# Kernel optimization log

Measured on AMD Instinct MI355X. Metric: run time of the kernel, lower is better.

## Reference

```python
import jax, jax.numpy as jnp
import numpy as np

B, F, Q = 8192, 128, 64
H1, H2 = 256, 256
THRESHOLD = 0.95
EPS = 1e-12


def setup_inputs() -> dict:
    key = jax.random.key(0)
    ks = jax.random.split(key, 8)
    in_dim = F + 1 + Q  # raw + quantum + graph feature
    def lin(k, fan_in, fan_out):
        bound = 1.0 / np.sqrt(fan_in)
        kw, kb = jax.random.split(k)
        W = jax.random.uniform(kw, (fan_out, fan_in), jnp.float32, -bound, bound)
        b = jax.random.uniform(kb, (fan_out,), jnp.float32, -bound, bound)
        return W, b
    W1, b1 = lin(ks[2], in_dim, H1)
    W2, b2 = lin(ks[3], H1, H2)
    W3, b3 = lin(ks[4], H2, 1)
    return {
        'x': jax.random.normal(ks[0], (B, F), jnp.float32),
        'quantum_features': jax.random.normal(ks[1], (B, Q), jnp.float32),
        'W1': W1, 'b1': b1, 'W2': W2, 'b2': b2, 'W3': W3, 'b3': b3,
    }


def _graph_feat(x):
    # normalized Gram matrix -> squared cosine fidelity -> threshold -> row mean
    xn = x / (jnp.linalg.norm(x, axis=1, keepdims=True) + EPS)  # [B, F]
    fid = jnp.square(xn @ xn.T)                                  # [B, B]
    adj = jnp.where(fid >= THRESHOLD, 1.0, 0.0)
    adj = adj * (1.0 - jnp.eye(x.shape[0], dtype=x.dtype))       # no self-edges
    return jnp.mean(adj, axis=1, keepdims=True)                  # [B, 1]


def reference(x, quantum_features, W1, b1, W2, b2, W3, b3):
    graph_feat = jax.lax.stop_gradient(_graph_feat(x))  # built under no_grad in torch
    feats = jnp.concatenate([x, quantum_features, graph_feat], axis=1)  # [B, F+Q+1]
    h = jax.nn.relu(feats @ W1.T + b1)
    h = jax.nn.relu(h @ W2.T + b2)
    out = h @ W3.T + b3  # [B, 1]
    return out[:, 0]
```

## Files before the change

kernel.cpp:

```cpp
#include <hip/hip_runtime.h>
#include <hip/hip_bf16.h>

typedef __attribute__((ext_vector_type(8))) short bf16x8;
typedef __attribute__((ext_vector_type(4))) float f32x4;
typedef unsigned int uint;

#define NROWS 8192
#define F_DIM 128
#define Q_DIM 64
#define KPAD  224
#define H_DIM 256

static __device__ inline unsigned short bf_bits(__hip_bfloat16 b) {
  unsigned short u; __builtin_memcpy(&u, &b, 2); return u;
}
static __device__ inline uint packhl(float v) {
  __hip_bfloat16 h = __float2bfloat16(v);
  float hf = __bfloat162float(h);
  __hip_bfloat16 l = __float2bfloat16(v - hf);
  return ((uint)bf_bits(l) << 16) | (uint)bf_bits(h);
}

__global__ __launch_bounds__(256) void norm_feats_kernel(const float* __restrict__ x,
                                                         const float* __restrict__ q,
                                                         __hip_bfloat16* __restrict__ xn,
                                                         uint* __restrict__ feats_p,
                                                         int* __restrict__ cnt) {
  int tid = threadIdx.x;
  int lane = tid & 63;
  int row = blockIdx.x * 4 + (tid >> 6);
  if (blockIdx.x < 32) cnt[blockIdx.x * 256 + tid] = 0;
  const float2 v = *(const float2*)(x + (size_t)row * F_DIM + lane * 2);
  float s = v.x * v.x + v.y * v.y;
#pragma unroll
  for (int off = 32; off; off >>= 1) s += __shfl_xor(s, off);
  float inv = 1.0f / (sqrtf(s) + 1e-12f);
  __hip_bfloat162 p;
  p.x = __float2bfloat16(v.x * inv);
  p.y = __float2bfloat16(v.y * inv);
  *(__hip_bfloat162*)(xn + (size_t)row * F_DIM + lane * 2) = p;

  uint* frow = feats_p + (size_t)row * KPAD;
  uint2 u;
  u.x = packhl(v.x); u.y = packhl(v.y);
  *(uint2*)(frow + lane * 2) = u;
  if (lane < 32) {
    const float2 qv = *(const float2*)(q + (size_t)row * Q_DIM + lane * 2);
    u.x = packhl(qv.x); u.y = packhl(qv.y);
    *(uint2*)(frow + 128 + lane * 2) = u;
  } else if (lane < 48) {
    uint2 z = {0u, 0u};
    *(uint2*)(frow + 192 + (lane - 32) * 2) = z;
  }
}

__global__ __launch_bounds__(256) void prep_w_kernel(const float* __restrict__ W1,
                                                     const float* __restrict__ W2,
                                                     uint* __restrict__ W1P,
                                                     uint* __restrict__ W2P) {
  int b = blockIdx.x, k = threadIdx.x;
  if (b < 256) {
    if (k < KPAD) W1P[b * KPAD + k] = (k < 193) ? packhl(W1[b * 193 + k]) : 0u;
  } else {
    int n = b - 256;
    W2P[n * 256 + k] = packhl(W2[n * 256 + k]);
  }
}

__global__ __launch_bounds__(256) void gram_kernel(const __hip_bfloat16* __restrict__ xnp,
                                                   int* __restrict__ cnt) {
  __shared__ char smem[65536];
  const short* xn = (const short*)xnp;
  int tid = threadIdx.x;
  int lane = tid & 63;
  int wave = tid >> 6;
  int lr = lane & 15;
  int quad = lane >> 4;

  int t = blockIdx.x;
  int bi = (int)((129.0f - sqrtf(129.0f * 129.0f - 8.0f * (float)t)) * 0.5f);
  while ((bi + 1) * (129 - (bi + 1)) / 2 <= t) bi++;
  while (bi * (129 - bi) / 2 > t) bi--;
  int bj = bi + (t - bi * (129 - bi) / 2);
  int i0 = bi * 128, j0 = bj * 128;

#pragma unroll
  for (int it = 0; it < 16; ++it) {
    int half = it >> 3;
    int row = (it & 7) * 16 + (tid >> 4);
    int chunk = tid & 15;
    int grow = (half ? j0 : i0) + row;
    bf16x8 v = *(const bf16x8*)(xn + (size_t)grow * F_DIM + chunk * 8);
    *(bf16x8*)(smem + half * 32768 + row * 256 + ((chunk ^ (row & 15)) << 4)) = v;
  }
  __syncthreads();

  int wi = (wave >> 1) * 64, wj = (wave & 1) * 64;

  f32x4 acc[4][4];
#pragma unroll
  for (int i = 0; i < 4; i++)
#pragma unroll
    for (int j = 0; j < 4; j++) acc[i][j] = (f32x4){0.f, 0.f, 0.f, 0.f};

#pragma unroll
  for (int kk = 0; kk < 4; kk++) {
    int c = kk * 4 + quad;
    bf16x8 a[4], b[4];
#pragma unroll
    for (int tt = 0; tt < 4; tt++) {
      int row = wi + tt * 16 + lr;
      a[tt] = *(const bf16x8*)(smem + row * 256 + ((c ^ lr) << 4));
    }
#pragma unroll
    for (int tt = 0; tt < 4; tt++) {
      int row = wj + tt * 16 + lr;
      b[tt] = *(const bf16x8*)(smem + 32768 + row * 256 + ((c ^ lr) << 4));
    }
#pragma unroll
    for (int tr = 0; tr < 4; tr++)
#pragma unroll
      for (int tc = 0; tc < 4; tc++)
        acc[tr][tc] = __builtin_amdgcn_mfma_f32_16x16x32_bf16(a[tr], b[tc], acc[tr][tc], 0, 0, 0);
  }

  int i_base = i0 + wi, j_base = j0 + wj;
  bool diag_wave = (i_base == j_base);
  bool offdiag_block = (bi != bj);

  float mx = 0.f;
#pragma unroll
  for (int tr = 0; tr < 4; tr++)
#pragma unroll
    for (int tc = 0; tc < 4; tc++)
#pragma unroll
      for (int r = 0; r < 4; r++) {
        float v = acc[tr][tc][r];
        if (diag_wave && tr == tc && lr == quad * 4 + r) v = 0.f;
        mx = fmaxf(mx, fabsf(v));
      }
  if (__any(mx >= 0.9746f)) {
    for (int tr = 0; tr < 4; tr++)
      for (int tc = 0; tc < 4; tc++)
        for (int r = 0; r < 4; r++) {
          float v = acc[tr][tc][r];
          int row = i_base + tr * 16 + quad * 4 + r;
          int col = j_base + tc * 16 + lr;
          if (v * v >= 0.95f && row != col) {
            atomicAdd(&cnt[row], 1);
            if (offdiag_block) atomicAdd(&cnt[col], 1);
          }
        }
  }
}

__global__ __launch_bounds__(256) void gf_kernel(const int* __restrict__ cnt,
                                                 const float* __restrict__ b3,
                                                 uint* __restrict__ feats_p,
                                                 float* __restrict__ out) {
  int i = blockIdx.x * 256 + threadIdx.x;
  feats_p[(size_t)i * KPAD + 192] = packhl((float)cnt[i] * (1.0f / 8192.0f));
  out[i] = b3[0];
}

template <int K, int MODE>
__global__ __launch_bounds__(256) void gemm_mfma(const uint* __restrict__ A,
                                                 const uint* __restrict__ Bp,
                                                 const float* __restrict__ bias,
                                                 uint* __restrict__ Out,
                                                 const float* __restrict__ W3,
                                                 float* __restrict__ out) {
  __shared__ short Ahi[128 * 40];
  __shared__ short Alo[128 * 40];
  __shared__ short Bhi[64 * 40];
  __shared__ short Blo[64 * 40];

  int tid = threadIdx.x;
  int lane = tid & 63;
  int wave = tid >> 6;
  int lr = lane & 15;
  int quad = lane >> 4;
  int mb = blockIdx.x * 128;
  int nb = blockIdx.y * 64;
  int wm = (wave & 1) * 64;
  int wn = (wave >> 1) * 32;

  int a_row = tid >> 3;
  int a_c4 = (tid & 7) * 4;
  int b_row = tid >> 3;

  f32x4 acc[4][2];
#pragma unroll
  for (int i = 0; i < 4; i++)
#pragma unroll
    for (int j = 0; j < 2; j++) acc[i][j] = (f32x4){0.f, 0.f, 0.f, 0.f};

  constexpr int NIT = K / 32;
  uint4 ar[4], br[2];

#pragma unroll
  for (int i = 0; i < 4; i++)
    ar[i] = *(const uint4*)(A + (size_t)(mb + a_row + i * 32) * K + a_c4);
#pragma unroll
  for (int i = 0; i < 2; i++)
    br[i] = *(const uint4*)(Bp + (size_t)(nb + b_row + i * 32) * K + a_c4);

  for (int it = 0; it < NIT; ++it) {
    __syncthreads();
#pragma unroll
    for (int i = 0; i < 4; i++) {
      int r = a_row + i * 32;
      uint h01 = (ar[i].x & 0xffffu) | (ar[i].y << 16);
      uint h23 = (ar[i].z & 0xffffu) | (ar[i].w << 16);
      uint l01 = (ar[i].x >> 16) | (ar[i].y & 0xffff0000u);
      uint l23 = (ar[i].z >> 16) | (ar[i].w & 0xffff0000u);
      *(uint2*)&Ahi[r * 40 + a_c4] = (uint2){h01, h23};
      *(uint2*)&Alo[r * 40 + a_c4] = (uint2){l01, l23};
    }
#pragma unroll
    for (int i = 0; i < 2; i++) {
      int r = b_row + i * 32;
      uint h01 = (br[i].x & 0xffffu) | (br[i].y << 16);
      uint h23 = (br[i].z & 0xffffu) | (br[i].w << 16);
      uint l01 = (br[i].x >> 16) | (br[i].y & 0xffff0000u);
      uint l23 = (br[i].z >> 16) | (br[i].w & 0xffff0000u);
      *(uint2*)&Bhi[r * 40 + a_c4] = (uint2){h01, h23};
      *(uint2*)&Blo[r * 40 + a_c4] = (uint2){l01, l23};
    }
    __syncthreads();

    if (it + 1 < NIT) {
      int k0 = (it + 1) * 32;
#pragma unroll
      for (int i = 0; i < 4; i++)
        ar[i] = *(const uint4*)(A + (size_t)(mb + a_row + i * 32) * K + k0 + a_c4);
#pragma unroll
      for (int i = 0; i < 2; i++)
        br[i] = *(const uint4*)(Bp + (size_t)(nb + b_row + i * 32) * K + k0 + a_c4);
    }

    bf16x8 ahi[4], alo[4], bhi[2], blo[2];
#pragma unroll
    for (int tt = 0; tt < 4; tt++) {
      int r = wm + tt * 16 + lr;
      ahi[tt] = *(const bf16x8*)&Ahi[r * 40 + quad * 8];
      alo[tt] = *(const bf16x8*)&Alo[r * 40 + quad * 8];
    }
#pragma unroll
    for (int tc = 0; tc < 2; tc++) {
      int r = wn + tc * 16 + lr;
      bhi[tc] = *(const bf16x8*)&Bhi[r * 40 + quad * 8];
      blo[tc] = *(const bf16x8*)&Blo[r * 40 + quad * 8];
    }
#pragma unroll
    for (int tt = 0; tt < 4; tt++)
#pragma unroll
      for (int tc = 0; tc < 2; tc++) {
        acc[tt][tc] = __builtin_amdgcn_mfma_f32_16x16x32_bf16(ahi[tt], bhi[tc], acc[tt][tc], 0, 0, 0);
        acc[tt][tc] = __builtin_amdgcn_mfma_f32_16x16x32_bf16(ahi[tt], blo[tc], acc[tt][tc], 0, 0, 0);
        acc[tt][tc] = __builtin_amdgcn_mfma_f32_16x16x32_bf16(alo[tt], bhi[tc], acc[tt][tc], 0, 0, 0);
      }
  }

  if (MODE == 1) {
#pragma unroll
    for (int tc = 0; tc < 2; tc++) {
      int n = nb + wn + tc * 16 + lr;
      float bv = bias[n];
#pragma unroll
      for (int tt = 0; tt < 4; tt++) {
        int m0 = mb + wm + tt * 16 + quad * 4;
#pragma unroll
        for (int r = 0; r < 4; r++) {
          float v = fmaxf(acc[tt][tc][r] + bv, 0.f);
          Out[(size_t)(m0 + r) * 256 + n] = packhl(v);
        }
      }
    }
  } else {
#pragma unroll
    for (int tt = 0; tt < 4; tt++) {
      float s[4] = {0.f, 0.f, 0.f, 0.f};
#pragma unroll
      for (int tc = 0; tc < 2; tc++) {
        int n = nb + wn + tc * 16 + lr;
        float bv = bias[n];
        float w3v = W3[n];
#pragma unroll
        for (int r = 0; r < 4; r++) {
          float v = fmaxf(acc[tt][tc][r] + bv, 0.f);
          s[r] += v * w3v;
        }
      }
#pragma unroll
      for (int r = 0; r < 4; r++) {
        s[r] += __shfl_xor(s[r], 1);
        s[r] += __shfl_xor(s[r], 2);
        s[r] += __shfl_xor(s[r], 4);
        s[r] += __shfl_xor(s[r], 8);
      }
      if (lr == 0) {
        int m0 = mb + wm + tt * 16 + quad * 4;
#pragma unroll
        for (int r = 0; r < 4; r++) atomicAdd(&out[m0 + r], s[r]);
      }
    }
  }
}

extern "C" void kernel_launch(void* const* d_in, const int* in_sizes, int n_in,
                              void* d_out, int out_size, void* d_ws, size_t ws_size,
                              hipStream_t stream) {
  const float* x  = (const float*)d_in[0];
  const float* q  = (const float*)d_in[1];
  const float* W1 = (const float*)d_in[2];
  const float* b1 = (const float*)d_in[3];
  const float* W2 = (const float*)d_in[4];
  const float* b2 = (const float*)d_in[5];
  const float* W3 = (const float*)d_in[6];
  const float* b3 = (const float*)d_in[7];
  float* out = (float*)d_out;

  char* ws = (char*)d_ws;
  __hip_bfloat16* xn = (__hip_bfloat16*)(ws);
  int*  cnt     = (int*)(ws + 0x200000);
  uint* W1P     = (uint*)(ws + 0x210000);
  uint* W2P     = (uint*)(ws + 0x250000);
  uint* feats_p = (uint*)(ws + 0x290000);
  uint* h1p     = (uint*)(ws + 0x990000);

  norm_feats_kernel<<<dim3(2048), dim3(256), 0, stream>>>(x, q, xn, feats_p, cnt);
  prep_w_kernel<<<dim3(512), dim3(256), 0, stream>>>(W1, W2, W1P, W2P);
  gram_kernel<<<dim3(2080), dim3(256), 0, stream>>>(xn, cnt);
  gf_kernel<<<dim3(32), dim3(256), 0, stream>>>(cnt, b3, feats_p, out);
  gemm_mfma<KPAD, 1><<<dim3(64, 4), dim3(256), 0, stream>>>(feats_p, W1P, b1, h1p, nullptr, nullptr);
  gemm_mfma<256, 2><<<dim3(64, 4), dim3(256), 0, stream>>>(h1p, W2P, b2, nullptr, W3, out);
}
```

Baseline: 111.7 us.

## Use FP8 scaled MFMA for Gram matrix and fuse prep/gf kernels

Normalized x is now quantized to FP8 (e4m3) and the Gram kernel uses the 16x16x128 scaled f8f6f4 MFMA, halving LDS and global traffic and issuing one MFMA per tile instead of four. The weight-prep kernel is merged into the normalization kernel. The graph-feature kernel is removed: the count is injected into the first GEMM's A tile, and b3 is added in the second GEMM's epilogue after a memset of out. The goal is fewer launches and a cheaper Gram pass. The risk is FP8 precision near the 0.95 fidelity threshold, where counts could differ from the reference.

```diff
diff --git a/kernel.cpp b/kernel.cpp
--- a/kernel.cpp
+++ b/kernel.cpp
@@ -2,6 +2,7 @@
 #include <hip/hip_bf16.h>
 
 typedef __attribute__((ext_vector_type(8))) short bf16x8;
+typedef __attribute__((ext_vector_type(8))) int i32x8;
 typedef __attribute__((ext_vector_type(4))) float f32x4;
 typedef unsigned int uint;
 
@@ -21,12 +22,26 @@
   return ((uint)bf_bits(l) << 16) | (uint)bf_bits(h);
 }
 
-__global__ __launch_bounds__(256) void norm_feats_kernel(const float* __restrict__ x,
-                                                         const float* __restrict__ q,
-                                                         __hip_bfloat16* __restrict__ xn,
-                                                         uint* __restrict__ feats_p,
-                                                         int* __restrict__ cnt) {
+__global__ __launch_bounds__(256) void norm_prep_kernel(const float* __restrict__ x,
+                                                        const float* __restrict__ q,
+                                                        const float* __restrict__ W1,
+                                                        const float* __restrict__ W2,
+                                                        unsigned char* __restrict__ xn8,
+                                                        uint* __restrict__ feats_p,
+                                                        uint* __restrict__ W1P,
+                                                        uint* __restrict__ W2P,
+                                                        int* __restrict__ cnt) {
   int tid = threadIdx.x;
+  if (blockIdx.x >= 2048) {
+    int b = blockIdx.x - 2048;
+    if (b < 256) {
+      if (tid < KPAD) W1P[b * KPAD + tid] = (tid < 193) ? packhl(W1[b * 193 + tid]) : 0u;
+    } else {
+      int n = b - 256;
+      W2P[n * 256 + tid] = packhl(W2[n * 256 + tid]);
+    }
+    return;
+  }
   int lane = tid & 63;
   int row = blockIdx.x * 4 + (tid >> 6);
   if (blockIdx.x < 32) cnt[blockIdx.x * 256 + tid] = 0;
@@ -35,10 +50,8 @@
 #pragma unroll
   for (int off = 32; off; off >>= 1) s += __shfl_xor(s, off);
   float inv = 1.0f / (sqrtf(s) + 1e-12f);
-  __hip_bfloat162 p;
-  p.x = __float2bfloat16(v.x * inv);
-  p.y = __float2bfloat16(v.y * inv);
-  *(__hip_bfloat162*)(xn + (size_t)row * F_DIM + lane * 2) = p;
+  int pk = __builtin_amdgcn_cvt_pk_fp8_f32(v.x * inv, v.y * inv, 0, 0);
+  *(unsigned short*)(xn8 + (size_t)row * F_DIM + lane * 2) = (unsigned short)(pk & 0xffff);
 
   uint* frow = feats_p + (size_t)row * KPAD;
   uint2 u;
@@ -54,23 +67,9 @@
   }
 }
 
-__global__ __launch_bounds__(256) void prep_w_kernel(const float* __restrict__ W1,
-                                                     const float* __restrict__ W2,
-                                                     uint* __restrict__ W1P,
-                                                     uint* __restrict__ W2P) {
-  int b = blockIdx.x, k = threadIdx.x;
-  if (b < 256) {
-    if (k < KPAD) W1P[b * KPAD + k] = (k < 193) ? packhl(W1[b * 193 + k]) : 0u;
-  } else {
-    int n = b - 256;
-    W2P[n * 256 + k] = packhl(W2[n * 256 + k]);
-  }
-}
-
-__global__ __launch_bounds__(256) void gram_kernel(const __hip_bfloat16* __restrict__ xnp,
-                                                   int* __restrict__ cnt) {
-  __shared__ char smem[65536];
-  const short* xn = (const short*)xnp;
+__global__ __launch_bounds__(256) void gram8_kernel(const unsigned char* __restrict__ xn8,
+                                                    int* __restrict__ cnt) {
+  __shared__ char smem[32768];
   int tid = threadIdx.x;
   int lane = tid & 63;
   int wave = tid >> 6;
@@ -85,13 +84,13 @@
   int i0 = bi * 128, j0 = bj * 128;
 
 #pragma unroll
-  for (int it = 0; it < 16; ++it) {
-    int half = it >> 3;
-    int row = (it & 7) * 16 + (tid >> 4);
-    int chunk = tid & 15;
+  for (int it = 0; it < 8; ++it) {
+    int half = it >> 2;
+    int row = (it & 3) * 32 + (tid >> 3);
+    int chunk = tid & 7;
     int grow = (half ? j0 : i0) + row;
-    bf16x8 v = *(const bf16x8*)(xn + (size_t)grow * F_DIM + chunk * 8);
-    *(bf16x8*)(smem + half * 32768 + row * 256 + ((chunk ^ (row & 15)) << 4)) = v;
+    uint4 v = *(const uint4*)(xn8 + (size_t)grow * F_DIM + chunk * 16);
+    *(uint4*)(smem + half * 16384 + row * 128 + ((chunk ^ (row & 7)) << 4)) = v;
   }
   __syncthreads();
 
@@ -103,26 +102,36 @@
 #pragma unroll
     for (int j = 0; j < 4; j++) acc[i][j] = (f32x4){0.f, 0.f, 0.f, 0.f};
 
-#pragma unroll
-  for (int kk = 0; kk < 4; kk++) {
-    int c = kk * 4 + quad;
-    bf16x8 a[4], b[4];
-#pragma unroll
-    for (int tt = 0; tt < 4; tt++) {
-      int row = wi + tt * 16 + lr;
-      a[tt] = *(const bf16x8*)(smem + row * 256 + ((c ^ lr) << 4));
-    }
-#pragma unroll
-    for (int tt = 0; tt < 4; tt++) {
-      int row = wj + tt * 16 + lr;
-      b[tt] = *(const bf16x8*)(smem + 32768 + row * 256 + ((c ^ lr) << 4));
-    }
-#pragma unroll
-    for (int tr = 0; tr < 4; tr++)
-#pragma unroll
-      for (int tc = 0; tc < 4; tc++)
-        acc[tr][tc] = __builtin_amdgcn_mfma_f32_16x16x32_bf16(a[tr], b[tc], acc[tr][tc], 0, 0, 0);
-  }
+  i32x8 a[4], b[4];
+#pragma unroll
+  for (int tt = 0; tt < 4; tt++) {
+    int r = wi + tt * 16 + lr;
+    const char* base = smem + r * 128;
+    uint4 lo = *(const uint4*)(base + (((2 * quad) ^ (r & 7)) << 4));
+    uint4 hi = *(const uint4*)(base + (((2 * quad + 1) ^ (r & 7)) << 4));
+    i32x8 f;
+    f[0] = lo.x; f[1] = lo.y; f[2] = lo.z; f[3] = lo.w;
+    f[4] = hi.x; f[5] = hi.y; f[6] = hi.z; f[7] = hi.w;
+    a[tt] = f;
+  }
+#pragma unroll
+  for (int tt = 0; tt < 4; tt++) {
+    int r = wj + tt * 16 + lr;
+    const char* base = smem + 16384 + r * 128;
+    uint4 lo = *(const uint4*)(base + (((2 * quad) ^ (r & 7)) << 4));
+    uint4 hi = *(const uint4*)(base + (((2 * quad + 1) ^ (r & 7)) << 4));
+    i32x8 f;
+    f[0] = lo.x; f[1] = lo.y; f[2] = lo.z; f[3] = lo.w;
+    f[4] = hi.x; f[5] = hi.y; f[6] = hi.z; f[7] = hi.w;
+    b[tt] = f;
+  }
+
+#pragma unroll
+  for (int tr = 0; tr < 4; tr++)
+#pragma unroll
+    for (int tc = 0; tc < 4; tc++)
+      acc[tr][tc] = __builtin_amdgcn_mfma_scale_f32_16x16x128_f8f6f4(
+          a[tr], b[tc], acc[tr][tc], 0, 0, 0, 0x7f7f7f7f, 0, 0x7f7f7f7f);
 
   int i_base = i0 + wi, j_base = j0 + wj;
   bool diag_wave = (i_base == j_base);
@@ -154,21 +163,14 @@
   }
 }
 
-__global__ __launch_bounds__(256) void gf_kernel(const int* __restrict__ cnt,
-                                                 const float* __restrict__ b3,
-                                                 uint* __restrict__ feats_p,
-                                                 float* __restrict__ out) {
-  int i = blockIdx.x * 256 + threadIdx.x;
-  feats_p[(size_t)i * KPAD + 192] = packhl((float)cnt[i] * (1.0f / 8192.0f));
-  out[i] = b3[0];
-}
-
 template <int K, int MODE>
 __global__ __launch_bounds__(256) void gemm_mfma(const uint* __restrict__ A,
                                                  const uint* __restrict__ Bp,
                                                  const float* __restrict__ bias,
                                                  uint* __restrict__ Out,
                                                  const float* __restrict__ W3,
+                                                 const float* __restrict__ b3,
+                                                 const int* __restrict__ cnt,
                                                  float* __restrict__ out) {
   __shared__ short Ahi[128 * 40];
   __shared__ short Alo[128 * 40];
@@ -187,7 +189,13 @@
 
   int a_row = tid >> 3;
   int a_c4 = (tid & 7) * 4;
-  int b_row = tid >> 3;
+
+  uint gf[4];
+  if (MODE == 1 && a_c4 == 0) {
+#pragma unroll
+    for (int i = 0; i < 4; i++)
+      gf[i] = packhl((float)cnt[mb + a_row + i * 32] * (1.0f / 8192.0f));
+  }
 
   f32x4 acc[4][2];
 #pragma unroll
@@ -203,9 +211,13 @@
     ar[i] = *(const uint4*)(A + (size_t)(mb + a_row + i * 32) * K + a_c4);
 #pragma unroll
   for (int i = 0; i < 2; i++)
-    br[i] = *(const uint4*)(Bp + (size_t)(nb + b_row + i * 32) * K + a_c4);
+    br[i] = *(const uint4*)(Bp + (size_t)(nb + a_row + i * 32) * K + a_c4);
 
   for (int it = 0; it < NIT; ++it) {
+    if (MODE == 1 && it == 6 && a_c4 == 0) {
+#pragma unroll
+      for (int i = 0; i < 4; i++) ar[i].x = gf[i];
+    }
     __syncthreads();
 #pragma unroll
     for (int i = 0; i < 4; i++) {
@@ -219,7 +231,7 @@
     }
 #pragma unroll
     for (int i = 0; i < 2; i++) {
-      int r = b_row + i * 32;
+      int r = a_row + i * 32;
       uint h01 = (br[i].x & 0xffffu) | (br[i].y << 16);
       uint h23 = (br[i].z & 0xffffu) | (br[i].w << 16);
       uint l01 = (br[i].x >> 16) | (br[i].y & 0xffff0000u);
@@ -236,7 +248,7 @@
         ar[i] = *(const uint4*)(A + (size_t)(mb + a_row + i * 32) * K + k0 + a_c4);
 #pragma unroll
       for (int i = 0; i < 2; i++)
-        br[i] = *(const uint4*)(Bp + (size_t)(nb + b_row + i * 32) * K + k0 + a_c4);
+        br[i] = *(const uint4*)(Bp + (size_t)(nb + a_row + i * 32) * K + k0 + a_c4);
     }
 
     bf16x8 ahi[4], alo[4], bhi[2], blo[2];
@@ -278,6 +290,7 @@
       }
     }
   } else {
+    float b3v = (blockIdx.y == 0 && wn == 0) ? b3[0] : 0.f;
 #pragma unroll
     for (int tt = 0; tt < 4; tt++) {
       float s[4] = {0.f, 0.f, 0.f, 0.f};
@@ -302,7 +315,7 @@
       if (lr == 0) {
         int m0 = mb + wm + tt * 16 + quad * 4;
 #pragma unroll
-        for (int r = 0; r < 4; r++) atomicAdd(&out[m0 + r], s[r]);
+        for (int r = 0; r < 4; r++) atomicAdd(&out[m0 + r], s[r] + b3v);
       }
     }
   }
@@ -322,17 +335,16 @@
   float* out = (float*)d_out;
 
   char* ws = (char*)d_ws;
-  __hip_bfloat16* xn = (__hip_bfloat16*)(ws);
-  int*  cnt     = (int*)(ws + 0x200000);
-  uint* W1P     = (uint*)(ws + 0x210000);
-  uint* W2P     = (uint*)(ws + 0x250000);
-  uint* feats_p = (uint*)(ws + 0x290000);
-  uint* h1p     = (uint*)(ws + 0x990000);
-
-  norm_feats_kernel<<<dim3(2048), dim3(256), 0, stream>>>(x, q, xn, feats_p, cnt);
-  prep_w_kernel<<<dim3(512), dim3(256), 0, stream>>>(W1, W2, W1P, W2P);
-  gram_kernel<<<dim3(2080), dim3(256), 0, stream>>>(xn, cnt);
-  gf_kernel<<<dim3(32), dim3(256), 0, stream>>>(cnt, b3, feats_p, out);
-  gemm_mfma<KPAD, 1><<<dim3(64, 4), dim3(256), 0, stream>>>(feats_p, W1P, b1, h1p, nullptr, nullptr);
-  gemm_mfma<256, 2><<<dim3(64, 4), dim3(256), 0, stream>>>(h1p, W2P, b2, nullptr, W3, out);
-}
+  unsigned char* xn8 = (unsigned char*)(ws);
+  int*  cnt     = (int*)(ws + 0x100000);
+  uint* W1P     = (uint*)(ws + 0x110000);
+  uint* W2P     = (uint*)(ws + 0x150000);
+  uint* feats_p = (uint*)(ws + 0x190000);
+  uint* h1p     = (uint*)(ws + 0x890000);
+
+  hipMemsetAsync(d_out, 0, (size_t)out_size * 4, stream);
+  norm_prep_kernel<<<dim3(2560), dim3(256), 0, stream>>>(x, q, W1, W2, xn8, feats_p, W1P, W2P, cnt);
+  gram8_kernel<<<dim3(2080), dim3(256), 0, stream>>>(xn8, cnt);
+  gemm_mfma<KPAD, 1><<<dim3(64, 4), dim3(256), 0, stream>>>(feats_p, W1P, b1, h1p, nullptr, nullptr, cnt, nullptr);
+  gemm_mfma<256, 2><<<dim3(64, 4), dim3(256), 0, stream>>>(h1p, W2P, b2, nullptr, W3, b3, nullptr, out);
+}
```

Result: faster. 103.8 us (-7.1%).
